# Performance work log

Hardware: AMD Instinct MI355X
Metric: run time of the kernel (lower is better)

Reference implementation:

```python
import jax, jax.numpy as jnp
import numpy as np
from math import log2

FPS = 100.0
MIN_BPM = 55.0
MAX_BPM = 215.0
NUM_TEMPI = 60
NUM_BEATS = 4
TRANS_LAMBDA = 100.0
OBS_LAMBDA = 16.0
NUM_FRAMES = 6000


def _intervals():
    mi = 60.0 * FPS / MAX_BPM
    ma = 60.0 * FPS / MIN_BPM
    iv = np.arange(round(mi), round(ma) + 1)
    if NUM_TEMPI < len(iv):
        n = NUM_TEMPI
        iv = np.zeros(0)
        while len(iv) < NUM_TEMPI:
            iv = np.unique(np.round(np.logspace(log2(mi), log2(ma), n, base=2)))
            n += 1
    return iv.astype(np.int64)


def _state_space():
    iv = _intervals()                      # (I,) tempo intervals in frames
    nsb = int(iv.sum())                    # states per beat
    first = np.concatenate([[0], np.cumsum(iv)[:-1]]).astype(np.int64)
    last = (np.cumsum(iv) - 1).astype(np.int64)
    pos_b = np.concatenate([np.arange(i) / float(i) for i in iv])
    positions = np.concatenate([pos_b + b for b in range(NUM_BEATS)])  # (S,)
    first_states = np.stack([first + b * nsb for b in range(NUM_BEATS)])  # (B,I)
    last_states = np.stack([last + b * nsb for b in range(NUM_BEATS)])    # (B,I)
    # exponential tempo transition (madmom exponential_transition, norm=True)
    ratio = iv[None, :].astype(np.float64) / iv[:, None].astype(np.float64)
    prob = np.exp(-TRANS_LAMBDA * np.abs(ratio - 1.0))
    prob[prob <= np.spacing(1)] = 0.0
    prob /= prob.sum(axis=1, keepdims=True)
    log_t = np.where(prob > 0, np.log(np.maximum(prob, 1e-300)), -1e30).astype(np.float32)
    log_trans = np.tile(log_t[None], (NUM_BEATS, 1, 1))  # same lambda per beat boundary
    prev_last = np.stack([last_states[(b - 1) % NUM_BEATS] for b in range(NUM_BEATS)])
    # observation pointers: 0 = no beat, 1 = beat, 2 = downbeat
    frac = positions % 1.0
    beat_idx = np.floor(positions).astype(np.int64)
    ptr = np.where(frac < 1.0 / OBS_LAMBDA, np.where(beat_idx == 0, 2, 1), 0)
    return first_states, prev_last, log_trans, ptr, nsb * NUM_BEATS


def setup_inputs() -> dict:
    key = jax.random.key(0)
    first_states, prev_last, log_trans, pointer, S = _state_space()
    # beat/downbeat activation probabilities; scaled so beat+downbeat < 1
    acts = jax.random.uniform(key, (NUM_FRAMES, 2), dtype=jnp.float32) * 0.45
    return {
        "activations": acts,
        "log_trans": jnp.asarray(log_trans),
        "prev_last": jnp.asarray(prev_last, dtype=jnp.int32),
        "first_states": jnp.asarray(first_states, dtype=jnp.int32),
        "pointer": jnp.asarray(pointer, dtype=jnp.int32),
        "num_states": S,
    }


def reference(activations, log_trans, prev_last, first_states, pointer, num_states):
    S = int(num_states)
    NEG = jnp.float32(-1e30)
    a_b = activations[:, 0]
    a_d = activations[:, 1]
    # log observation densities: [no-beat, beat, downbeat], shape (F, 3)
    dens = jnp.stack([
        jnp.log((1.0 - a_b - a_d) / (OBS_LAMBDA - 1.0)),
        jnp.log(a_b),
        jnp.log(a_d),
    ], axis=1)
    first_flat = first_states.reshape(-1)  # (B*I,)
    base_ptr = jnp.arange(S, dtype=jnp.int32) - 1  # default predecessor s-1

    def step(v, dens_t):
        # within-interval advance: state s comes from s-1 with prob 1
        v_shift = jnp.concatenate([jnp.full((1,), NEG, v.dtype), v[:-1]])
        # beat boundaries: first states of beat b from last states of beat b-1
        cand = v[prev_last]                      # (B, I)
        scores = cand[:, :, None] + log_trans    # (B, I_from, I_to)
        best = scores.max(axis=1).reshape(-1)    # (B*I,)
        arg = scores.argmax(axis=1)              # (B, I_to)
        bp_first = jnp.take_along_axis(prev_last, arg.astype(jnp.int32), axis=1).reshape(-1)
        ptr = base_ptr.at[first_flat].set(bp_first)
        v_new = v_shift.at[first_flat].set(best) + dens_t[pointer]
        return v_new, ptr

    v0 = jnp.full((S,), -jnp.log(jnp.float32(S)))  # uniform initial distribution
    v_final, bps = jax.lax.scan(step, v0, dens)    # bps: (F, S) backpointers
    last_state = jnp.argmax(v_final).astype(jnp.int32)
    logp = v_final[last_state]

    def back(s, bp_t):
        p = bp_t[s]
        return p, p

    _, earlier = jax.lax.scan(back, last_state, bps[1:], reverse=True)
    path = jnp.concatenate([earlier, last_state[None]])  # (F,) best state sequence
    return path, logp
```

## Files before the change

### kernel.cpp

```cpp
#include <hip/hip_runtime.h>
#include <stdint.h>


#define NB 4
#define KF 15
#define QW 16
#define NPMAX 256
#define TBATCH 32
#define NEGV -1.0e30f

__device__ __forceinline__ float bf16u_to_f(uint16_t u) {
    union { uint32_t i; float f; } v; v.i = ((uint32_t)u) << 16; return v.f;
}

template<int CTRL>
__device__ __forceinline__ int dpp_i(int x) {
    return __builtin_amdgcn_update_dpp(0, x, CTRL, 0xF, 0xF, true);
}
template<int CTRL>
__device__ __forceinline__ float dpp_f(float x) {
    return __int_as_float(dpp_i<CTRL>(__float_as_int(x)));
}

__device__ __forceinline__ void load_acts(const void* p, int isbf, int t, float& a, float& d) {
    if (isbf) {
        const uint16_t* u = (const uint16_t*)p;
        uint32_t w = *(const uint32_t*)(u + 2 * t);
        a = bf16u_to_f((uint16_t)w); d = bf16u_to_f((uint16_t)(w >> 16));
    } else {
        const float2* f = (const float2*)p;
        float2 v = f[t]; a = v.x; d = v.y;
    }
}

__global__ __launch_bounds__(1024) void dbn_viterbi_v2(
    const void* __restrict__ acts_raw,
    const void* __restrict__ lt_raw,
    const int*  __restrict__ prev_last,
    const int*  __restrict__ first_states,
    float*      __restrict__ out,
    float*      __restrict__ ws_lastv,
    float*      __restrict__ ws_dens,
    int T, int S, int F)
{
    const int tid  = (int)threadIdx.x;
    const int NP   = NB * T;
    const int lane = tid & 63;
    const int wvx  = tid >> 6;

    __shared__ alignas(16) float lring[32 * 256];
    __shared__ alignas(16) float densr[64 * 4];
    __shared__ float bestv[NPMAX];
    __shared__ float bound[16];
    __shared__ int   fsld[NPMAX];
    __shared__ int   plds[NPMAX];
    __shared__ int   pref[NPMAX + 1];
    __shared__ float wvs[16];
    __shared__ int   wss[16];
    __shared__ int   flag_s, mspan_s;

    if (tid == 0) {
        const uint16_t* au = (const uint16_t*)acts_raw;
        int bf = 1;
        for (int i = 0; i < 32; i++) {
            uint16_t e = au[2 * i];
            uint8_t h8 = (uint8_t)(e >> 8);
            if (!(e == 0 || (h8 >= 0x20 && h8 < 0x40))) bf = 0;
        }
        flag_s = bf; mspan_s = 0;
    }
    if (tid < NP) { fsld[tid] = first_states[tid]; plds[tid] = prev_last[tid]; }
    for (int i = tid; i < 32 * 256; i += 1024) lring[i] = NEGV;
    __syncthreads();
    const int isbf = flag_s;
    const int nsb  = S / NB;
    const uint16_t* lt_u = (const uint16_t*)lt_raw;
    const float*    lt_f = (const float*)lt_raw;

    for (int f = tid; f < F; f += 1024) {
        float ab, ad;
        load_acts(acts_raw, isbf, f, ab, ad);
        float4 r;
        r.x = logf(((1.0f - ab) - ad) / 15.0f);
        r.y = logf(ab);
        r.z = logf(ad);
        r.w = 0.0f;
        *(float4*)&ws_dens[f * 4] = r;
    }
    __threadfence();

    if (tid == 0) {
        int acc = 0;
        for (int g = 0; g < NP; g++) {
            int b = g / T, ib = g - b * T;
            int end = (ib + 1 < T) ? fsld[g + 1] : (b + 1) * nsb;
            int L = end - fsld[g];
            pref[g] = acc; acc += (L + KF - 1) / KF;
        }
        pref[NP] = acc;
    }
    __syncthreads();
    const int NT = pref[NP];

    const bool act_u = (tid < NT);
    int g_own = 0, startg = 0, Lg = 1, sb = 0, lq = 0;
    bool is_last = false, pv2 = false;
    if (act_u) {
        int lo = 0, hi = NP - 1;
        while (lo < hi) { int mid = (lo + hi + 1) >> 1; if (pref[mid] <= tid) lo = mid; else hi = mid - 1; }
        g_own = lo;
        int j = tid - pref[lo];
        int b = g_own / T, ib = g_own - b * T;
        startg = fsld[g_own];
        int end = (ib + 1 < T) ? fsld[g_own + 1] : (b + 1) * nsb;
        Lg = end - startg;
        int n = (Lg + KF - 1) / KF;
        sb = startg + Lg - KF * (n - j);
        is_last = (j == n - 1);
        lq = (b << 6) + ib;
        pv2 = (b == 0);
    }
    bool hb[KF], hq[KF];
    #pragma unroll
    for (int kk = 0; kk < KF; kk++) {
        int i = sb + kk - startg;
        hq[kk] = act_u && (i <= 0);
        hb[kk] = act_u && (16 * i < Lg);
    }

    const int g_a = tid >> 2, k4 = tid & 3;
    const bool act_g = (g_a < NP);
    int rowbase = 0, lo_b = 0;
    int b_a = 0, j_a = 0;
    if (act_g) {
        b_a = g_a / T; j_a = g_a - b_a * T;
        rowbase = ((b_a + 3) & 3) << 6;
        int lo = T, hi = 0;
        for (int i = 0; i < T; i++) {
            int idx = (b_a * T + i) * T + j_a;
            float v = isbf ? bf16u_to_f(lt_u[idx]) : lt_f[idx];
            if (v > -1e29f) { if (i < lo) lo = i; hi = i; }
        }
        lo_b = lo;
        if (k4 == 0) atomicMax(&mspan_s, hi - lo + 1);
    }
    __syncthreads();
    const bool banded = (mspan_s <= 44);
    float ltreg[QW];
    #pragma unroll
    for (int u = 0; u < QW; u++) ltreg[u] = NEGV;
    int cb = 0;
    if (act_g) {
        if (banded) {
            cb = (lo_b & ~3) + 12 * k4;
            if (cb > 52) cb = 52;
        } else {
            cb = 16 * k4;
        }
        const int nu = banded ? 12 : 16;
        for (int u = 0; u < nu; u++) {
            int i = cb + u;
            if (i < T) {
                int idx = (b_a * T + i) * T + j_a;
                ltreg[u] = isbf ? bf16u_to_f(lt_u[idx]) : lt_f[idx];
            }
        }
    }

    const float vinit = -logf((float)S);
    float vreg[KF];
    #pragma unroll
    for (int kk = 0; kk < KF; kk++) vreg[kk] = vinit;
    if (act_u && is_last) lring[(31 << 8) + lq] = vinit;
    if (lane == 63) bound[wvx] = vinit;
    float inc_pipe = vinit;
    if (tid < 64 && tid < F) {
        float4 r = *(const float4*)&ws_dens[tid * 4];
        *(float4*)&densr[tid * 4] = r;
    }

    const int WQ = NP >> 2;
    const int TQ = T >> 2;

    for (int t = 0; t < F; t++) {
        __syncthreads();
        const float* lvR = &lring[((t + 31) & 31) << 8];
        float inc_use = inc_pipe;
        if (lane == 0) inc_use = bound[(wvx + 15) & 15];

        if (wvx == 15) {
            if ((t & 31) == 0 && t >= 32 && lane < 32) {
                int fr = t + 32 + lane;
                if (fr < F) {
                    float4 r = *(const float4*)&ws_dens[fr * 4];
                    *(float4*)&densr[(fr & 63) * 4] = r;
                }
            }
            if ((t & 15) == 0 && t > 0 && lane < WQ) {
                int c = lane;
                int beat = c / TQ;
                int srcoff = 4 * c + 4 * beat;
                int t0 = t - 16;
                for (int r2 = 0; r2 < 16; r2++) {
                    int row = t0 + r2;
                    float4 v4 = *(const float4*)&lring[((row & 31) << 8) + srcoff];
                    *(float4*)&ws_lastv[(size_t)row * NP + 4 * c] = v4;
                }
            }
        } else if (act_g) {
            const float* rowp = lvR + rowbase + cb;
            if (banded) {
                float4 l0 = *(const float4*)(rowp + 0);
                float4 l1 = *(const float4*)(rowp + 4);
                float4 l2 = *(const float4*)(rowp + 8);
                float m0 = fmaxf(fmaxf(l0.x + ltreg[0], l0.y + ltreg[1]),
                                 fmaxf(l0.z + ltreg[2], l0.w + ltreg[3]));
                float m1 = fmaxf(fmaxf(l1.x + ltreg[4], l1.y + ltreg[5]),
                                 fmaxf(l1.z + ltreg[6], l1.w + ltreg[7]));
                float m2 = fmaxf(fmaxf(l2.x + ltreg[8], l2.y + ltreg[9]),
                                 fmaxf(l2.z + ltreg[10], l2.w + ltreg[11]));
                float mv = fmaxf(fmaxf(m0, m1), m2);
                mv = fmaxf(mv, dpp_f<0xB1>(mv));
                mv = fmaxf(mv, dpp_f<0x4E>(mv));
                if (k4 == 0) bestv[g_a] = mv;
            } else {
                float4 l0 = *(const float4*)(rowp + 0);
                float4 l1 = *(const float4*)(rowp + 4);
                float4 l2 = *(const float4*)(rowp + 8);
                float4 l3 = *(const float4*)(rowp + 12);
                float m0 = fmaxf(fmaxf(l0.x + ltreg[0], l0.y + ltreg[1]),
                                 fmaxf(l0.z + ltreg[2], l0.w + ltreg[3]));
                float m1 = fmaxf(fmaxf(l1.x + ltreg[4], l1.y + ltreg[5]),
                                 fmaxf(l1.z + ltreg[6], l1.w + ltreg[7]));
                float m2 = fmaxf(fmaxf(l2.x + ltreg[8], l2.y + ltreg[9]),
                                 fmaxf(l2.z + ltreg[10], l2.w + ltreg[11]));
                float m3 = fmaxf(fmaxf(l3.x + ltreg[12], l3.y + ltreg[13]),
                                 fmaxf(l3.z + ltreg[14], l3.w + ltreg[15]));
                float mv = fmaxf(fmaxf(m0, m1), fmaxf(m2, m3));
                mv = fmaxf(mv, dpp_f<0xB1>(mv));
                mv = fmaxf(mv, dpp_f<0x4E>(mv));
                if (k4 == 0) bestv[g_a] = mv;
            }
        }

        __syncthreads();
        int doff = (t & 63) << 2;
        float d0  = densr[doff];
        float dpv = densr[doff + (pv2 ? 2 : 1)];
        float bq  = bestv[g_own];
        #pragma unroll
        for (int kk = KF - 1; kk >= 0; kk--) {
            float prev = (kk == 0) ? inc_use : vreg[kk - 1];
            prev = hq[kk] ? bq : prev;
            float add = hb[kk] ? dpv : d0;
            vreg[kk] = prev + add;
        }
        if (act_u && is_last) lring[((t & 31) << 8) + lq] = vreg[KF - 1];
        if (lane == 63) bound[wvx] = vreg[KF - 1];
        inc_pipe = __shfl_up(vreg[KF - 1], 1, 64);
    }

    __syncthreads();
    if (wvx == 15 && lane < WQ) {
        int lastf = (F - 1) & ~15;
        int c = lane;
        int beat = c / TQ;
        int srcoff = 4 * c + 4 * beat;
        for (int row = lastf; row <= F - 2; row++) {
            float4 v4 = *(const float4*)&lring[((row & 31) << 8) + srcoff];
            *(float4*)&ws_lastv[(size_t)row * NP + 4 * c] = v4;
        }
        __threadfence();
    }

    float mv = -INFINITY; int ms = 0x7FFFFFFF;
    #pragma unroll
    for (int kk = 0; kk < KF; kk++) {
        int s = sb + kk;
        bool valid = act_u && (s >= startg);
        float v = vreg[kk];
        if (valid && v > mv) { mv = v; ms = s; }
    }
    #pragma unroll
    for (int d = 1; d < 64; d <<= 1) {
        float ov = __shfl_xor(mv, d, 64);
        int   os = __shfl_xor(ms, d, 64);
        if (ov > mv || (ov == mv && os < ms)) { mv = ov; ms = os; }
    }
    if (lane == 0) { wvs[wvx] = mv; wss[wvx] = ms; }
    __syncthreads();

    if (tid == 0) {
        float bm = -INFINITY; int bs = 0x7FFFFFFF;
        for (int w = 0; w < 16; w++) {
            if (wvs[w] > bm || (wvs[w] == bm && wss[w] < bs)) { bm = wvs[w]; bs = wss[w]; }
        }
        int s = bs;
        int t = F - 1;
        out[F - 1] = (float)s;
        while (t > 0) {
            int b = s / nsb;
            int lo = b * T, hi = b * T + T - 1;
            while (lo < hi) { int mid = (lo + hi + 1) >> 1; if (fsld[mid] <= s) lo = mid; else hi = mid - 1; }
            int p = lo;
            int run = s - fsld[p];
            if (run == 0) {
                int jt = p - b * T;
                int pb = (b + 3) & 3;
                const float* lrow = &ws_lastv[(size_t)(t - 1) * NP + pb * T];
                float bmv = -INFINITY; int ai = 0;
                for (int i = 0; i < T; i++) {
                    int idx = (b * T + i) * T + jt;
                    float ltv = isbf ? bf16u_to_f(lt_u[idx]) : lt_f[idx];
                    float sc = lrow[i] + ltv;
                    if (sc > bmv) { bmv = sc; ai = i; }
                }
                s = plds[b * T + ai];
                out[t - 1] = (float)s;
                t--;
            } else {
                int m = (run < t) ? run : t;
                for (int jj = 0; jj < m; jj++) out[t - 1 - jj] = (float)(s - 1 - jj);
                s -= m; t -= m;
            }
        }
        out[F] = bm;
    }
}

template<bool FAST>
__global__ __launch_bounds__(1024) void dbn_viterbi_kernel(
    const void* __restrict__ acts_raw, const void* __restrict__ lt_raw,
    const int* __restrict__ prev_last, const int* __restrict__ first_states,
    float* __restrict__ out, float* __restrict__ ws_lastv, uint8_t* __restrict__ ws_argi,
    int T, int S, int F)
{
    const int tid  = (int)threadIdx.x;
    const int NP   = NB * T;
    const int lane = tid & 63;
    const int wvx  = tid >> 6;

    __shared__ alignas(16) float lastv2[2 * NB * 64];
    __shared__ float bestv[NPMAX];
    __shared__ float bound[16];
    __shared__ int   fsld[NPMAX];
    __shared__ int   plds[NPMAX];
    __shared__ int   pref[NPMAX + 1];
    __shared__ float dens_s[4];
    __shared__ float wvs[16];
    __shared__ int   wss[16];
    __shared__ int   flag_s;
    __shared__ uint8_t argi_s[TBATCH * 240 + 16];

    if (tid == 0) {
        const uint16_t* au = (const uint16_t*)acts_raw;
        int bf = 1;
        for (int i = 0; i < 32; i++) {
            uint16_t e = au[2 * i];
            uint8_t h8 = (uint8_t)(e >> 8);
            if (!(e == 0 || (h8 >= 0x20 && h8 < 0x40))) bf = 0;
        }
        flag_s = bf;
    }
    if (tid < NP)          { fsld[tid] = first_states[tid]; plds[tid] = prev_last[tid]; }
    if (tid < 2 * NB * 64) lastv2[tid] = NEGV;
    __syncthreads();
    const int isbf = flag_s;
    const int nsb  = S / NB;
    const uint16_t* lt_u = (const uint16_t*)lt_raw;
    const float*    lt_f = (const float*)lt_raw;

    if (tid == 0) {
        int acc = 0;
        for (int g = 0; g < NP; g++) {
            int b = g / T, ib = g - b * T;
            int end = (ib + 1 < T) ? fsld[g + 1] : (b + 1) * nsb;
            int L = end - fsld[g];
            pref[g] = acc; acc += (L + KF - 1) / KF;
        }
        pref[NP] = acc;
    }
    __syncthreads();
    const int NT = pref[NP];

    const bool act_u = (tid < NT);
    int g_own = 0, startg = 0, Lg = 1, sb = 0, lq = 0;
    bool is_last = false, pv2 = false;
    if (act_u) {
        int lo = 0, hi = NP - 1;
        while (lo < hi) { int mid = (lo + hi + 1) >> 1; if (pref[mid] <= tid) lo = mid; else hi = mid - 1; }
        g_own = lo;
        int j = tid - pref[lo];
        int b = g_own / T, ib = g_own - b * T;
        startg = fsld[g_own];
        int end = (ib + 1 < T) ? fsld[g_own + 1] : (b + 1) * nsb;
        Lg = end - startg;
        int n = (Lg + KF - 1) / KF;
        sb = startg + Lg - KF * (n - j);
        is_last = (j == n - 1);
        lq = (b << 6) + ib;
        pv2 = (b == 0);
    }
    bool hb[KF], hq[KF];
    #pragma unroll
    for (int kk = 0; kk < KF; kk++) {
        int i = sb + kk - startg;
        hq[kk] = act_u && (i <= 0);
        hb[kk] = act_u && (16 * i < Lg);
    }

    const int g_a = tid >> 2, k4 = tid & 3;
    const bool act_g = (g_a < NP);
    float ltreg[QW];
    #pragma unroll
    for (int u = 0; u < QW; u++) ltreg[u] = NEGV;
    int rowbase = 0;
    if (act_g) {
        int b = g_a / T, j = g_a - (g_a / T) * T;
        rowbase = ((b + 3) & 3) << 6;
        #pragma unroll
        for (int u = 0; u < QW; u++) {
            int i = k4 * QW + u;
            if (i < T) {
                int idx = (b * T + i) * T + j;
                ltreg[u] = isbf ? bf16u_to_f(lt_u[idx]) : lt_f[idx];
            }
        }
    }

    const float vinit = -logf((float)S);
    float vreg[KF];
    #pragma unroll
    for (int kk = 0; kk < KF; kk++) vreg[kk] = vinit;
    if (act_u && is_last) lastv2[256 + lq] = vinit;
    if (lane == 63) bound[wvx] = vinit;
    float inc_pipe = vinit;
    float ab_c = 0.0f, ad_c = 0.0f;
    if (wvx == 15 && lane >= 60 && lane < 63) load_acts(acts_raw, isbf, 0, ab_c, ad_c);

    for (int t = 0; t < F; t++) {
        __syncthreads();
        const float* lvR = lastv2 + (((t & 1) ^ 1) << 8);
        float inc_use = inc_pipe;
        if (lane == 0) inc_use = bound[(wvx + 15) & 15];

        if (wvx == 15) {
            if (lane >= 60 && lane < 63) {
                int c3 = lane - 60;
                float dv = (c3 == 0) ? logf(((1.0f - ab_c) - ad_c) / 15.0f)
                         : (c3 == 1) ? logf(ab_c) : logf(ad_c);
                dens_s[c3] = dv;
                if (t + 1 < F) load_acts(acts_raw, isbf, t + 1, ab_c, ad_c);
            }
        } else if (act_g) {
            const float* rowp = &lvR[rowbase + k4 * QW];
            float4 l0 = *(const float4*)(rowp + 0);
            float4 l1 = *(const float4*)(rowp + 4);
            float4 l2 = *(const float4*)(rowp + 8);
            float4 l3 = *(const float4*)(rowp + 12);
            if (FAST) {
                float m0 = fmaxf(fmaxf(l0.x + ltreg[0],  l0.y + ltreg[1]),
                                 fmaxf(l0.z + ltreg[2],  l0.w + ltreg[3]));
                float m1 = fmaxf(fmaxf(l1.x + ltreg[4],  l1.y + ltreg[5]),
                                 fmaxf(l1.z + ltreg[6],  l1.w + ltreg[7]));
                float m2 = fmaxf(fmaxf(l2.x + ltreg[8],  l2.y + ltreg[9]),
                                 fmaxf(l2.z + ltreg[10], l2.w + ltreg[11]));
                float m3 = fmaxf(fmaxf(l3.x + ltreg[12], l3.y + ltreg[13]),
                                 fmaxf(l3.z + ltreg[14], l3.w + ltreg[15]));
                float mv = fmaxf(fmaxf(m0, m1), fmaxf(m2, m3));
                mv = fmaxf(mv, dpp_f<0xB1>(mv));
                mv = fmaxf(mv, dpp_f<0x4E>(mv));
                if (k4 == 0) bestv[g_a] = mv;
            } else {
                float cand[QW] = { l0.x, l0.y, l0.z, l0.w, l1.x, l1.y, l1.z, l1.w,
                                   l2.x, l2.y, l2.z, l2.w, l3.x, l3.y, l3.z, l3.w };
                float mv = -INFINITY; int ai = 0;
                #pragma unroll
                for (int u = 0; u < QW; u++) {
                    float sc = cand[u] + ltreg[u];
                    if (sc > mv) { mv = sc; ai = k4 * QW + u; }
                }
                float ov = dpp_f<0xB1>(mv); int oa = dpp_i<0xB1>(ai);
                if (ov > mv || (ov == mv && oa < ai)) { mv = ov; ai = oa; }
                ov = dpp_f<0x4E>(mv); oa = dpp_i<0x4E>(ai);
                if (ov > mv || (ov == mv && oa < ai)) { mv = ov; ai = oa; }
                if (k4 == 0) {
                    bestv[g_a] = mv;
                    argi_s[(t & (TBATCH - 1)) * NP + g_a] = (uint8_t)ai;
                }
            }
        }

        __syncthreads();
        float d0  = dens_s[0];
        float dpv = pv2 ? dens_s[2] : dens_s[1];
        float bq  = bestv[g_own];
        #pragma unroll
        for (int kk = KF - 1; kk >= 0; kk--) {
            float prev = (kk == 0) ? inc_use : vreg[kk - 1];
            prev = hq[kk] ? bq : prev;
            float add = hb[kk] ? dpv : d0;
            vreg[kk] = prev + add;
        }
        float* lvW = lastv2 + ((t & 1) << 8);
        if (act_u && is_last) lvW[lq] = vreg[KF - 1];
        if (lane == 63) bound[wvx] = vreg[KF - 1];
        inc_pipe = __shfl_up(vreg[KF - 1], 1, 64);

        if (FAST) {
            if (wvx == 15 && t > 0 && lane < (NP >> 2)) {
                int c = lane << 2;
                int bb = c / T, cib = c - bb * T;
                float4 v4 = *(const float4*)&lvR[(bb << 6) + cib];
                *(float4*)&ws_lastv[(size_t)(t - 1) * NP + c] = v4;
            }
        } else {
            int tB = t & (TBATCH - 1);
            if (tB == TBATCH - 1 || t == F - 1) {
                int nbytes = (tB + 1) * NP;
                int t0 = t - tB;
                for (int off = tid * 4; off < nbytes; off += 4096) {
                    uint32_t w = *(const uint32_t*)&argi_s[off];
                    *(uint32_t*)&ws_argi[(size_t)t0 * NP + off] = w;
                }
            }
        }
    }

    __syncthreads();
    float mv = -INFINITY; int ms = 0x7FFFFFFF;
    #pragma unroll
    for (int kk = 0; kk < KF; kk++) {
        int s = sb + kk;
        bool valid = act_u && (s >= startg);
        float v = vreg[kk];
        if (valid && v > mv) { mv = v; ms = s; }
    }
    #pragma unroll
    for (int d = 1; d < 64; d <<= 1) {
        float ov = __shfl_xor(mv, d, 64);
        int   os = __shfl_xor(ms, d, 64);
        if (ov > mv || (ov == mv && os < ms)) { mv = ov; ms = os; }
    }
    if (lane == 0) { wvs[wvx] = mv; wss[wvx] = ms; }
    __syncthreads();

    if (tid == 0) {
        float bm = -INFINITY; int bs = 0x7FFFFFFF;
        for (int w = 0; w < 16; w++) {
            if (wvs[w] > bm || (wvs[w] == bm && wss[w] < bs)) { bm = wvs[w]; bs = wss[w]; }
        }
        int s = bs;
        int t = F - 1;
        out[F - 1] = (float)s;
        while (t > 0) {
            int b = s / nsb;
            int lo = b * T, hi = b * T + T - 1;
            while (lo < hi) { int mid = (lo + hi + 1) >> 1; if (fsld[mid] <= s) lo = mid; else hi = mid - 1; }
            int p = lo;
            int run = s - fsld[p];
            if (run == 0) {
                int ai;
                if (FAST) {
                    int jt = p - b * T;
                    int pb = (b + 3) & 3;
                    const float* lrow = &ws_lastv[(size_t)(t - 1) * NP + pb * T];
                    float bmv = -INFINITY; ai = 0;
                    for (int i = 0; i < T; i++) {
                        int idx = (b * T + i) * T + jt;
                        float ltv = isbf ? bf16u_to_f(lt_u[idx]) : lt_f[idx];
                        float sc = lrow[i] + ltv;
                        if (sc > bmv) { bmv = sc; ai = i; }
                    }
                } else {
                    ai = ws_argi[(size_t)t * NP + p];
                }
                s = plds[b * T + ai];
                out[t - 1] = (float)s;
                t--;
            } else {
                int m = (run < t) ? run : t;
                for (int jj = 0; jj < m; jj++) out[t - 1 - jj] = (float)(s - 1 - jj);
                s -= m; t -= m;
            }
        }
        out[F] = bm;
    }
}

extern "C" void kernel_launch(void* const* d_in, const int* in_sizes, int n_in,
                              void* d_out, int out_size, void* d_ws, size_t ws_size,
                              hipStream_t stream) {
    const int F  = in_sizes[0] / 2;
    const int NP = in_sizes[2];
    const int T  = NP / NB;
    const int S  = in_sizes[4];

    const size_t need2 = ((size_t)F * NP + 4 * (size_t)F) * 4;
    const bool okgeom = ((T & 3) == 0) && (NP <= NPMAX) && (T <= 64) && (F >= 2);
    const bool fast2  = okgeom && (ws_size >= need2);
    const bool fast1  = okgeom && (ws_size >= (size_t)F * NP * 4);

    if (fast2) {
        float* ws_lv = (float*)d_ws;
        float* ws_de = ws_lv + (size_t)F * NP;
        hipLaunchKernelGGL(dbn_viterbi_v2, dim3(1), dim3(1024), 0, stream,
                           d_in[0], d_in[1],
                           (const int*)d_in[2], (const int*)d_in[3],
                           (float*)d_out, ws_lv, ws_de, T, S, F);
    } else if (fast1) {
        hipLaunchKernelGGL(dbn_viterbi_kernel<true>, dim3(1), dim3(1024), 0, stream,
                           d_in[0], d_in[1],
                           (const int*)d_in[2], (const int*)d_in[3],
                           (float*)d_out, (float*)d_ws, (uint8_t*)d_ws, T, S, F);
    } else {
        hipLaunchKernelGGL(dbn_viterbi_kernel<false>, dim3(1), dim3(1024), 0, stream,
                           d_in[0], d_in[1],
                           (const int*)d_in[2], (const int*)d_in[3],
                           (float*)d_out, (float*)d_ws, (uint8_t*)d_ws, T, S, F);
    }
}
```

Measured before the change: 6.212 ms.

## Fuse boundary max into owner threads and drop one barrier per frame

Each owner thread now computes the beat-boundary max itself over a 48-wide band of transition weights held in registers. This removes the separate 4-lanes-per-column reduction through shared memory (bestv) and the second __syncthreads per frame. The wave-boundary value is double-buffered by frame parity so a single barrier per step is enough. In exchange each owner does about 48 serial add-max operations and holds 48 extra registers per thread, which may hurt occupancy or lengthen the critical path. The unused fast1 template variant is also removed.

```diff
diff --git a/kernel.cpp b/kernel.cpp
--- a/kernel.cpp
+++ b/kernel.cpp
@@ -5,6 +5,7 @@
 #define NB 4
 #define KF 15
 #define QW 16
+#define BW 48
 #define NPMAX 256
 #define TBATCH 32
 #define NEGV -1.0e30f
@@ -33,7 +34,7 @@
     }
 }
 
-__global__ __launch_bounds__(1024) void dbn_viterbi_v2(
+__global__ __launch_bounds__(1024) void dbn_viterbi_v3(
     const void* __restrict__ acts_raw,
     const void* __restrict__ lt_raw,
     const int*  __restrict__ prev_last,
@@ -50,8 +51,7 @@
 
     __shared__ alignas(16) float lring[32 * 256];
     __shared__ alignas(16) float densr[64 * 4];
-    __shared__ float bestv[NPMAX];
-    __shared__ float bound[16];
+    __shared__ float bound2[32];
     __shared__ int   fsld[NPMAX];
     __shared__ int   plds[NPMAX];
     __shared__ int   pref[NPMAX + 1];
@@ -128,51 +128,37 @@
         hb[kk] = act_u && (16 * i < Lg);
     }
 
-    const int g_a = tid >> 2, k4 = tid & 3;
-    const bool act_g = (g_a < NP);
-    int rowbase = 0, lo_b = 0;
-    int b_a = 0, j_a = 0;
-    if (act_g) {
-        b_a = g_a / T; j_a = g_a - b_a * T;
-        rowbase = ((b_a + 3) & 3) << 6;
+    int rowbase = 0, c0 = 0, colbase = 0;
+    float ltb[BW];
+    #pragma unroll
+    for (int u = 0; u < BW; u++) ltb[u] = NEGV;
+    if (act_u) {
+        int b = g_own / T, j = g_own - (g_own / T) * T;
+        rowbase = ((b + 3) & 3) << 6;
+        colbase = b * T * T + j;
         int lo = T, hi = 0;
         for (int i = 0; i < T; i++) {
-            int idx = (b_a * T + i) * T + j_a;
-            float v = isbf ? bf16u_to_f(lt_u[idx]) : lt_f[idx];
-            if (v > -1e29f) { if (i < lo) lo = i; hi = i; }
-        }
-        lo_b = lo;
-        if (k4 == 0) atomicMax(&mspan_s, hi - lo + 1);
-    }
-    __syncthreads();
-    const bool banded = (mspan_s <= 44);
-    float ltreg[QW];
-    #pragma unroll
-    for (int u = 0; u < QW; u++) ltreg[u] = NEGV;
-    int cb = 0;
-    if (act_g) {
-        if (banded) {
-            cb = (lo_b & ~3) + 12 * k4;
-            if (cb > 52) cb = 52;
-        } else {
-            cb = 16 * k4;
-        }
-        const int nu = banded ? 12 : 16;
-        for (int u = 0; u < nu; u++) {
-            int i = cb + u;
-            if (i < T) {
-                int idx = (b_a * T + i) * T + j_a;
-                ltreg[u] = isbf ? bf16u_to_f(lt_u[idx]) : lt_f[idx];
-            }
-        }
-    }
+            float v = isbf ? bf16u_to_f(lt_u[colbase + i * T]) : lt_f[colbase + i * T];
+            if (v > -1e29f) { if (i < lo) lo = i; if (i > hi) hi = i; }
+        }
+        if (lo > hi) { lo = 0; hi = 0; }
+        atomicMax(&mspan_s, hi - lo + 1);
+        c0 = lo & ~3;
+        if (c0 + BW > 64) c0 = 64 - BW;
+        for (int u = 0; u < BW; u++) {
+            int i = c0 + u;
+            if (i < T) ltb[u] = isbf ? bf16u_to_f(lt_u[colbase + i * T]) : lt_f[colbase + i * T];
+        }
+    }
+    __syncthreads();
+    const bool narrow = (mspan_s <= BW);
 
     const float vinit = -logf((float)S);
     float vreg[KF];
     #pragma unroll
     for (int kk = 0; kk < KF; kk++) vreg[kk] = vinit;
     if (act_u && is_last) lring[(31 << 8) + lq] = vinit;
-    if (lane == 63) bound[wvx] = vinit;
+    if (lane == 63) bound2[16 + wvx] = vinit;
     float inc_pipe = vinit;
     if (tid < 64 && tid < F) {
         float4 r = *(const float4*)&ws_dens[tid * 4];
@@ -181,12 +167,12 @@
 
     const int WQ = NP >> 2;
     const int TQ = T >> 2;
+    __syncthreads();
 
     for (int t = 0; t < F; t++) {
-        __syncthreads();
         const float* lvR = &lring[((t + 31) & 31) << 8];
         float inc_use = inc_pipe;
-        if (lane == 0) inc_use = bound[(wvx + 15) & 15];
+        if (lane == 0) inc_use = bound2[(((t + 1) & 1) << 4) + ((wvx + 15) & 15)];
 
         if (wvx == 15) {
             if ((t & 31) == 0 && t >= 32 && lane < 32) {
@@ -207,47 +193,30 @@
                     *(float4*)&ws_lastv[(size_t)row * NP + 4 * c] = v4;
                 }
             }
-        } else if (act_g) {
-            const float* rowp = lvR + rowbase + cb;
-            if (banded) {
-                float4 l0 = *(const float4*)(rowp + 0);
-                float4 l1 = *(const float4*)(rowp + 4);
-                float4 l2 = *(const float4*)(rowp + 8);
-                float m0 = fmaxf(fmaxf(l0.x + ltreg[0], l0.y + ltreg[1]),
-                                 fmaxf(l0.z + ltreg[2], l0.w + ltreg[3]));
-                float m1 = fmaxf(fmaxf(l1.x + ltreg[4], l1.y + ltreg[5]),
-                                 fmaxf(l1.z + ltreg[6], l1.w + ltreg[7]));
-                float m2 = fmaxf(fmaxf(l2.x + ltreg[8], l2.y + ltreg[9]),
-                                 fmaxf(l2.z + ltreg[10], l2.w + ltreg[11]));
-                float mv = fmaxf(fmaxf(m0, m1), m2);
-                mv = fmaxf(mv, dpp_f<0xB1>(mv));
-                mv = fmaxf(mv, dpp_f<0x4E>(mv));
-                if (k4 == 0) bestv[g_a] = mv;
+        }
+
+        float bq = -INFINITY;
+        if (act_u) {
+            if (narrow) {
+                const float* rowp = lvR + rowbase + c0;
+                #pragma unroll
+                for (int q4 = 0; q4 < BW / 4; q4++) {
+                    float4 l = *(const float4*)(rowp + 4 * q4);
+                    float m = fmaxf(fmaxf(l.x + ltb[4 * q4 + 0], l.y + ltb[4 * q4 + 1]),
+                                    fmaxf(l.z + ltb[4 * q4 + 2], l.w + ltb[4 * q4 + 3]));
+                    bq = fmaxf(bq, m);
+                }
             } else {
-                float4 l0 = *(const float4*)(rowp + 0);
-                float4 l1 = *(const float4*)(rowp + 4);
-                float4 l2 = *(const float4*)(rowp + 8);
-                float4 l3 = *(const float4*)(rowp + 12);
-                float m0 = fmaxf(fmaxf(l0.x + ltreg[0], l0.y + ltreg[1]),
-                                 fmaxf(l0.z + ltreg[2], l0.w + ltreg[3]));
-                float m1 = fmaxf(fmaxf(l1.x + ltreg[4], l1.y + ltreg[5]),
-                                 fmaxf(l1.z + ltreg[6], l1.w + ltreg[7]));
-                float m2 = fmaxf(fmaxf(l2.x + ltreg[8], l2.y + ltreg[9]),
-                                 fmaxf(l2.z + ltreg[10], l2.w + ltreg[11]));
-                float m3 = fmaxf(fmaxf(l3.x + ltreg[12], l3.y + ltreg[13]),
-                                 fmaxf(l3.z + ltreg[14], l3.w + ltreg[15]));
-                float mv = fmaxf(fmaxf(m0, m1), fmaxf(m2, m3));
-                mv = fmaxf(mv, dpp_f<0xB1>(mv));
-                mv = fmaxf(mv, dpp_f<0x4E>(mv));
-                if (k4 == 0) bestv[g_a] = mv;
-            }
-        }
-
-        __syncthreads();
+                for (int i = 0; i < T; i++) {
+                    float ltv = isbf ? bf16u_to_f(lt_u[colbase + i * T]) : lt_f[colbase + i * T];
+                    bq = fmaxf(bq, lvR[rowbase + i] + ltv);
+                }
+            }
+        }
+
         int doff = (t & 63) << 2;
         float d0  = densr[doff];
         float dpv = densr[doff + (pv2 ? 2 : 1)];
-        float bq  = bestv[g_own];
         #pragma unroll
         for (int kk = KF - 1; kk >= 0; kk--) {
             float prev = (kk == 0) ? inc_use : vreg[kk - 1];
@@ -256,11 +225,12 @@
             vreg[kk] = prev + add;
         }
         if (act_u && is_last) lring[((t & 31) << 8) + lq] = vreg[KF - 1];
-        if (lane == 63) bound[wvx] = vreg[KF - 1];
+        if (lane == 63) bound2[((t & 1) << 4) + wvx] = vreg[KF - 1];
         inc_pipe = __shfl_up(vreg[KF - 1], 1, 64);
-    }
-
-    __syncthreads();
+
+        __syncthreads();
+    }
+
     if (wvx == 15 && lane < WQ) {
         int lastf = (F - 1) & ~15;
         int c = lane;
@@ -328,11 +298,10 @@
     }
 }
 
-template<bool FAST>
-__global__ __launch_bounds__(1024) void dbn_viterbi_kernel(
+__global__ __launch_bounds__(1024) void dbn_viterbi_v1(
     const void* __restrict__ acts_raw, const void* __restrict__ lt_raw,
     const int* __restrict__ prev_last, const int* __restrict__ first_states,
-    float* __restrict__ out, float* __restrict__ ws_lastv, uint8_t* __restrict__ ws_argi,
+    float* __restrict__ out, uint8_t* __restrict__ ws_argi,
     int T, int S, int F)
 {
     const int tid  = (int)threadIdx.x;
@@ -458,36 +427,21 @@
             float4 l1 = *(const float4*)(rowp + 4);
             float4 l2 = *(const float4*)(rowp + 8);
             float4 l3 = *(const float4*)(rowp + 12);
-            if (FAST) {
-                float m0 = fmaxf(fmaxf(l0.x + ltreg[0],  l0.y + ltreg[1]),
-                                 fmaxf(l0.z + ltreg[2],  l0.w + ltreg[3]));
-                float m1 = fmaxf(fmaxf(l1.x + ltreg[4],  l1.y + ltreg[5]),
-                                 fmaxf(l1.z + ltreg[6],  l1.w + ltreg[7]));
-                float m2 = fmaxf(fmaxf(l2.x + ltreg[8],  l2.y + ltreg[9]),
-                                 fmaxf(l2.z + ltreg[10], l2.w + ltreg[11]));
-                float m3 = fmaxf(fmaxf(l3.x + ltreg[12], l3.y + ltreg[13]),
-                                 fmaxf(l3.z + ltreg[14], l3.w + ltreg[15]));
-                float mv = fmaxf(fmaxf(m0, m1), fmaxf(m2, m3));
-                mv = fmaxf(mv, dpp_f<0xB1>(mv));
-                mv = fmaxf(mv, dpp_f<0x4E>(mv));
-                if (k4 == 0) bestv[g_a] = mv;
-            } else {
-                float cand[QW] = { l0.x, l0.y, l0.z, l0.w, l1.x, l1.y, l1.z, l1.w,
-                                   l2.x, l2.y, l2.z, l2.w, l3.x, l3.y, l3.z, l3.w };
-                float mv = -INFINITY; int ai = 0;
-                #pragma unroll
-                for (int u = 0; u < QW; u++) {
-                    float sc = cand[u] + ltreg[u];
-                    if (sc > mv) { mv = sc; ai = k4 * QW + u; }
-                }
-                float ov = dpp_f<0xB1>(mv); int oa = dpp_i<0xB1>(ai);
-                if (ov > mv || (ov == mv && oa < ai)) { mv = ov; ai = oa; }
-                ov = dpp_f<0x4E>(mv); oa = dpp_i<0x4E>(ai);
-                if (ov > mv || (ov == mv && oa < ai)) { mv = ov; ai = oa; }
-                if (k4 == 0) {
-                    bestv[g_a] = mv;
-                    argi_s[(t & (TBATCH - 1)) * NP + g_a] = (uint8_t)ai;
-                }
+            float cand[QW] = { l0.x, l0.y, l0.z, l0.w, l1.x, l1.y, l1.z, l1.w,
+                               l2.x, l2.y, l2.z, l2.w, l3.x, l3.y, l3.z, l3.w };
+            float mv = -INFINITY; int ai = 0;
+            #pragma unroll
+            for (int u = 0; u < QW; u++) {
+                float sc = cand[u] + ltreg[u];
+                if (sc > mv) { mv = sc; ai = k4 * QW + u; }
+            }
+            float ov = dpp_f<0xB1>(mv); int oa = dpp_i<0xB1>(ai);
+            if (ov > mv || (ov == mv && oa < ai)) { mv = ov; ai = oa; }
+            ov = dpp_f<0x4E>(mv); oa = dpp_i<0x4E>(ai);
+            if (ov > mv || (ov == mv && oa < ai)) { mv = ov; ai = oa; }
+            if (k4 == 0) {
+                bestv[g_a] = mv;
+                argi_s[(t & (TBATCH - 1)) * NP + g_a] = (uint8_t)ai;
             }
         }
 
@@ -507,22 +461,13 @@
         if (lane == 63) bound[wvx] = vreg[KF - 1];
         inc_pipe = __shfl_up(vreg[KF - 1], 1, 64);
 
-        if (FAST) {
-            if (wvx == 15 && t > 0 && lane < (NP >> 2)) {
-                int c = lane << 2;
-                int bb = c / T, cib = c - bb * T;
-                float4 v4 = *(const float4*)&lvR[(bb << 6) + cib];
-                *(float4*)&ws_lastv[(size_t)(t - 1) * NP + c] = v4;
-            }
-        } else {
-            int tB = t & (TBATCH - 1);
-            if (tB == TBATCH - 1 || t == F - 1) {
-                int nbytes = (tB + 1) * NP;
-                int t0 = t - tB;
-                for (int off = tid * 4; off < nbytes; off += 4096) {
-                    uint32_t w = *(const uint32_t*)&argi_s[off];
-                    *(uint32_t*)&ws_argi[(size_t)t0 * NP + off] = w;
-                }
+        int tB = t & (TBATCH - 1);
+        if (tB == TBATCH - 1 || t == F - 1) {
+            int nbytes = (tB + 1) * NP;
+            int t0 = t - tB;
+            for (int off = tid * 4; off < nbytes; off += 4096) {
+                uint32_t w = *(const uint32_t*)&argi_s[off];
+                *(uint32_t*)&ws_argi[(size_t)t0 * NP + off] = w;
             }
         }
     }
@@ -560,21 +505,7 @@
             int p = lo;
             int run = s - fsld[p];
             if (run == 0) {
-                int ai;
-                if (FAST) {
-                    int jt = p - b * T;
-                    int pb = (b + 3) & 3;
-                    const float* lrow = &ws_lastv[(size_t)(t - 1) * NP + pb * T];
-                    float bmv = -INFINITY; ai = 0;
-                    for (int i = 0; i < T; i++) {
-                        int idx = (b * T + i) * T + jt;
-                        float ltv = isbf ? bf16u_to_f(lt_u[idx]) : lt_f[idx];
-                        float sc = lrow[i] + ltv;
-                        if (sc > bmv) { bmv = sc; ai = i; }
-                    }
-                } else {
-                    ai = ws_argi[(size_t)t * NP + p];
-                }
+                int ai = ws_argi[(size_t)t * NP + p];
                 s = plds[b * T + ai];
                 out[t - 1] = (float)s;
                 t--;
@@ -596,27 +527,21 @@
     const int T  = NP / NB;
     const int S  = in_sizes[4];
 
-    const size_t need2 = ((size_t)F * NP + 4 * (size_t)F) * 4;
+    const size_t need3 = ((size_t)F * NP + 4 * (size_t)F) * 4;
     const bool okgeom = ((T & 3) == 0) && (NP <= NPMAX) && (T <= 64) && (F >= 2);
-    const bool fast2  = okgeom && (ws_size >= need2);
-    const bool fast1  = okgeom && (ws_size >= (size_t)F * NP * 4);
-
-    if (fast2) {
+    const bool fast3  = okgeom && (ws_size >= need3);
+
+    if (fast3) {
         float* ws_lv = (float*)d_ws;
         float* ws_de = ws_lv + (size_t)F * NP;
-        hipLaunchKernelGGL(dbn_viterbi_v2, dim3(1), dim3(1024), 0, stream,
+        hipLaunchKernelGGL(dbn_viterbi_v3, dim3(1), dim3(1024), 0, stream,
                            d_in[0], d_in[1],
                            (const int*)d_in[2], (const int*)d_in[3],
                            (float*)d_out, ws_lv, ws_de, T, S, F);
-    } else if (fast1) {
-        hipLaunchKernelGGL(dbn_viterbi_kernel<true>, dim3(1), dim3(1024), 0, stream,
+    } else {
+        hipLaunchKernelGGL(dbn_viterbi_v1, dim3(1), dim3(1024), 0, stream,
                            d_in[0], d_in[1],
                            (const int*)d_in[2], (const int*)d_in[3],
-                           (float*)d_out, (float*)d_ws, (uint8_t*)d_ws, T, S, F);
-    } else {
-        hipLaunchKernelGGL(dbn_viterbi_kernel<false>, dim3(1), dim3(1024), 0, stream,
-                           d_in[0], d_in[1],
-                           (const int*)d_in[2], (const int*)d_in[3],
-                           (float*)d_out, (float*)d_ws, (uint8_t*)d_ws, T, S, F);
-    }
-}
+                           (float*)d_out, (uint8_t*)d_ws, T, S, F);
+    }
+}
```

After: 7.222 ms. 1.16x slower.
